# Kernel tuning notes

Measured on AMD Instinct MI355X. Metric: run time of the kernel, lower is better.

The kernel has to match this reference:

```python
import jax, jax.numpy as jnp
import numpy as np

D_HEAD = 64
KV_GROUPS = 3
KSIZE = 7


def _win_idx(L, ksize):
    # NATTEN neighborhood: window centered at i, shifted to stay in-bounds.
    start = jnp.clip(jnp.arange(L) - ksize // 2, 0, L - ksize)  # [L]
    return start[:, None] + jnp.arange(ksize)[None, :]          # [L, k]


def _natten2d(q, k, v, ksize):
    # q,k,v: [n, nh, H, W, e]; q pre-scaled.
    H, W = q.shape[2], q.shape[3]
    ih = _win_idx(H, ksize)  # [H, k]
    iw = _win_idx(W, ksize)  # [W, k]
    # gather per-query key/value windows: [n, nh, H, W, k, k, e]
    kg = k[:, :, ih[:, None, :, None], iw[None, :, None, :], :]
    vg = v[:, :, ih[:, None, :, None], iw[None, :, None, :], :]
    logits = jnp.einsum('nhije,nhijabe->nhijab', q, kg)  # [n,nh,H,W,k,k]
    n_, nh = logits.shape[:2]
    a = jax.nn.softmax(logits.reshape(n_, nh, H, W, ksize * ksize), axis=-1)
    a = a.reshape(logits.shape)
    return jnp.einsum('nhijab,nhijabe->nhije', a, vg)  # [n,nh,H,W,e]


def _to_heads(p, nh, e):
    n, h, w, _ = p.shape
    return p.reshape(n, h, w, nh, e).transpose(0, 3, 1, 2, 4)  # [n,nh,h,w,e]


def setup_inputs() -> dict:
    key = jax.random.key(0)
    k1, k2, k3 = jax.random.split(key, 3)
    x = jax.random.normal(k1, (2, 32, 32, 768), dtype=jnp.float32)
    w_qkv = jax.random.normal(k2, (1280, 768), dtype=jnp.float32) * 0.02
    w_out = jax.random.normal(k3, (768, 768), dtype=jnp.float32) * 0.02
    return {"x": x, "w_qkv": w_qkv, "w_out": w_out}


def reference(x, w_qkv, w_out):
    n, H, W, d_model = x.shape
    q_heads = d_model // D_HEAD
    kv_heads = q_heads // KV_GROUPS
    qkv = x @ w_qkv.T  # [n,H,W,1280]
    q, k, v = jnp.split(
        qkv, [q_heads * D_HEAD, (q_heads + kv_heads) * D_HEAD], axis=-1)
    q = _to_heads(q, q_heads, D_HEAD)
    k = jnp.tile(_to_heads(k, kv_heads, D_HEAD), (1, KV_GROUPS, 1, 1, 1))
    v = jnp.tile(_to_heads(v, kv_heads, D_HEAD), (1, KV_GROUPS, 1, 1, 1))
    q = q / (D_HEAD ** 0.5)
    o = _natten2d(q, k, v, KSIZE)           # [n,nh,H,W,e]
    o = o.transpose(0, 2, 3, 1, 4).reshape(n, H, W, d_model)
    return o @ w_out.T
```

## Files before the change

### kernel.cpp

```cpp
#include <hip/hip_runtime.h>
#include <hip/hip_bf16.h>


typedef __attribute__((ext_vector_type(8))) __bf16 bf16x8;
typedef __attribute__((ext_vector_type(4))) float floatx4;
typedef unsigned short u16;

__device__ inline u16 f2bf(float f) {
    union { float f; unsigned u; } v; v.f = f;
    return (u16)((v.u + 0x7fff + ((v.u >> 16) & 1)) >> 16);
}

__device__ inline void gl_lds16(const void* g, void* l) {
    __builtin_amdgcn_global_load_lds(
        (const __attribute__((address_space(1))) void*)g,
        (__attribute__((address_space(3))) void*)l, 16, 0, 0);
}

__global__ __launch_bounds__(256) void convert_kernel(
    const float* __restrict__ x, const float* __restrict__ w1,
    const float* __restrict__ w2, u16* __restrict__ xb,
    u16* __restrict__ w1b, u16* __restrict__ w2b)
{
    int t = blockIdx.x * blockDim.x + threadIdx.x;
    const float* s; u16* d;
    if (t < 393216)      { s = x;  d = xb; }
    else if (t < 638976) { s = w1; d = w1b; t -= 393216; }
    else                 { s = w2; d = w2b; t -= 638976; }
    float4 v = ((const float4*)s)[t];
    ushort4 o;
    o.x = f2bf(v.x); o.y = f2bf(v.y); o.z = f2bf(v.z); o.w = f2bf(v.w);
    ((ushort4*)d)[t] = o;
}

template<int MODE>
__global__ __launch_bounds__(256) void gemm_nt(
    const u16* __restrict__ A, const u16* __restrict__ B,
    float* __restrict__ out, u16* __restrict__ Cq, u16* __restrict__ vT,
    int K)
{
    __shared__ __align__(16) u16 As[8 * 2048];
    __shared__ __align__(16) u16 Bs[8 * 2048];
    const int tid = threadIdx.x;
    const int lane = tid & 63;
    const int wave = tid >> 6;
    const int bm = blockIdx.y * 64;
    const int bn = blockIdx.x * 64;
    const int qr = (wave >> 1) * 32;
    const int qc = (wave & 1) * 32;

    floatx4 acc[2][2] = {};

    const u16* Xsrc = (wave < 2) ? A : B;
    const int   bx  = (wave < 2) ? bm : bn;
    u16* Xlds       = (wave < 2) ? As : Bs;
    const int half  = wave & 1;
    const int l2 = lane >> 2;
    const int l3 = (lane & 3) * 8;
    int gofs[16], lofs[16];
    #pragma unroll
    for (int cc = 0; cc < 16; cc++) {
        int c = half * 16 + cc, kc = c & 7, rg = c >> 3;
        gofs[cc] = (bx + rg * 16 + l2) * K + kc * 32 + l3;
        lofs[cc] = kc * 2048 + rg * 512;
    }

    const int fr = lane & 15;
    const int fk = (lane >> 4) * 8;

    for (int k0 = 0; k0 < K; k0 += 256) {
        #pragma unroll
        for (int cc = 0; cc < 16; cc++)
            gl_lds16(Xsrc + gofs[cc] + k0, Xlds + lofs[cc]);
        __syncthreads();
        #pragma unroll
        for (int kc = 0; kc < 8; kc++) {
            bf16x8 af0 = *(const bf16x8*)&As[kc * 2048 + (qr +      fr) * 32 + fk];
            bf16x8 af1 = *(const bf16x8*)&As[kc * 2048 + (qr + 16 + fr) * 32 + fk];
            bf16x8 bf0 = *(const bf16x8*)&Bs[kc * 2048 + (qc +      fr) * 32 + fk];
            bf16x8 bf1 = *(const bf16x8*)&Bs[kc * 2048 + (qc + 16 + fr) * 32 + fk];
            acc[0][0] = __builtin_amdgcn_mfma_f32_16x16x32_bf16(af0, bf0, acc[0][0], 0, 0, 0);
            acc[0][1] = __builtin_amdgcn_mfma_f32_16x16x32_bf16(af0, bf1, acc[0][1], 0, 0, 0);
            acc[1][0] = __builtin_amdgcn_mfma_f32_16x16x32_bf16(af1, bf0, acc[1][0], 0, 0, 0);
            acc[1][1] = __builtin_amdgcn_mfma_f32_16x16x32_bf16(af1, bf1, acc[1][1], 0, 0, 0);
        }
        __syncthreads();
    }

    const int cr = (lane >> 4) * 4;
    const int ccol = lane & 15;
    #pragma unroll
    for (int i = 0; i < 2; i++) {
        #pragma unroll
        for (int j = 0; j < 2; j++) {
            const int row0 = bm + qr + i * 16 + cr;
            const int col  = bn + qc + j * 16 + ccol;
            if (MODE == 0) {
                float4 w = {acc[i][j][0], acc[i][j][1], acc[i][j][2], acc[i][j][3]};
                *(float4*)&out[(size_t)col * 768 + row0] = w;
            } else {
                if (row0 < 1024) {
                    ushort4 w;
                    w.x = f2bf(acc[i][j][0]); w.y = f2bf(acc[i][j][1]);
                    w.z = f2bf(acc[i][j][2]); w.w = f2bf(acc[i][j][3]);
                    *(ushort4*)&Cq[(size_t)col * 1024 + row0] = w;
                } else {
                    #pragma unroll
                    for (int r = 0; r < 4; r++)
                        vT[(size_t)(row0 + r - 1024) * 2048 + col] = f2bf(acc[i][j][r]);
                }
            }
        }
    }
}

__global__ __launch_bounds__(256) void natten_mfma(
    const u16* __restrict__ qkv, const u16* __restrict__ vT,
    u16* __restrict__ o)
{
    __shared__ __align__(16) u16 Pw[4 * 512];
    const int h  = blockIdx.x;
    const int tb = blockIdx.y;
    const int g  = h & 3;
    const int batch = tb >> 4;
    const int ti = ((tb >> 2) & 3) * 8;
    const int tj = (tb & 3) * 8;
    const int wu_i = min(max(ti - 3, 0), 18);
    const int oj   = min(max(tj - 3, 0) & ~3, 16);
    const int lane = threadIdx.x & 63, wave = threadIdx.x >> 6;
    const int pixbase = batch << 10;

    const int fr = lane & 15;
    const int fk = (lane >> 4) * 8;

    bf16x8 aq0, aq1;
    {
        int qq = wave * 16 + fr;
        int pixq = pixbase + (ti + (qq >> 3)) * 32 + tj + (qq & 7);
        const u16* qp = &qkv[(size_t)pixq * 1024 + h * 64];
        aq0 = *(const bf16x8*)(qp + fk);
        aq1 = *(const bf16x8*)(qp + 32 + fk);
    }

    bool colok[4]; int tlo[4], thi[4];
    #pragma unroll
    for (int r = 0; r < 4; r++) {
        int qq = wave * 16 + (lane >> 4) * 4 + r;
        int qi = ti + (qq >> 3), qj = tj + (qq & 7);
        int si = min(max(qi - 3, 0), 25);
        int sj = min(max(qj - 3, 0), 25);
        colok[r] = (oj + fr >= sj) && (oj + fr <= sj + 6);
        tlo[r] = si - wu_i; thi[r] = tlo[r] + 6;
    }

    float s[14][4];
    float mx[4] = {-1e30f, -1e30f, -1e30f, -1e30f};
    #pragma unroll
    for (int t = 0; t < 14; t++) {
        int kp = pixbase + (wu_i + t) * 32 + oj + fr;
        const u16* krow = &qkv[(size_t)kp * 1024 + 768 + g * 64];
        bf16x8 bk0 = *(const bf16x8*)(krow + fk);
        bf16x8 bk1 = *(const bf16x8*)(krow + 32 + fk);
        floatx4 a4 = {};
        a4 = __builtin_amdgcn_mfma_f32_16x16x32_bf16(aq0, bk0, a4, 0, 0, 0);
        a4 = __builtin_amdgcn_mfma_f32_16x16x32_bf16(aq1, bk1, a4, 0, 0, 0);
        #pragma unroll
        for (int r = 0; r < 4; r++) {
            bool v = colok[r] && (t >= tlo[r]) && (t <= thi[r]);
            s[t][r] = v ? a4[r] * 0.125f : -1e30f;
            mx[r] = fmaxf(mx[r], s[t][r]);
        }
    }
    #pragma unroll
    for (int r = 0; r < 4; r++) {
        mx[r] = fmaxf(mx[r], __shfl_xor(mx[r], 1));
        mx[r] = fmaxf(mx[r], __shfl_xor(mx[r], 2));
        mx[r] = fmaxf(mx[r], __shfl_xor(mx[r], 4));
        mx[r] = fmaxf(mx[r], __shfl_xor(mx[r], 8));
    }
    float l[4] = {0.f, 0.f, 0.f, 0.f};
    #pragma unroll
    for (int t = 0; t < 14; t++)
        #pragma unroll
        for (int r = 0; r < 4; r++) {
            float p = __expf(s[t][r] - mx[r]);
            s[t][r] = p; l[r] += p;
        }
    #pragma unroll
    for (int r = 0; r < 4; r++) {
        l[r] += __shfl_xor(l[r], 1);
        l[r] += __shfl_xor(l[r], 2);
        l[r] += __shfl_xor(l[r], 4);
        l[r] += __shfl_xor(l[r], 8);
    }
    float rinv[4];
    #pragma unroll
    for (int r = 0; r < 4; r++) rinv[r] = 1.0f / l[r];

    u16* pw = &Pw[wave * 512];
    floatx4 oacc[4] = {};
    const int vrow = (fk >= 16) ? 1 : 0;
    const int vcol = oj + (fk & 8);
    #pragma unroll
    for (int kc = 0; kc < 7; kc++) {
        #pragma unroll
        for (int tt = 0; tt < 2; tt++) {
            int t = kc * 2 + tt;
            #pragma unroll
            for (int r = 0; r < 4; r++)
                pw[((lane >> 4) * 4 + r) * 32 + tt * 16 + fr] =
                    f2bf(s[t][r] * rinv[r]);
        }
        bf16x8 bp = *(const bf16x8*)&pw[fr * 32 + fk];
        const int vpix = pixbase + (wu_i + kc * 2 + vrow) * 32 + vcol;
        #pragma unroll
        for (int u = 0; u < 4; u++) {
            const u16* vp = &vT[(size_t)(g * 64 + u * 16 + fr) * 2048 + vpix];
            union { ushort4 q[2]; bf16x8 v; } av;
            av.q[0] = *(const ushort4*)vp;
            av.q[1] = *(const ushort4*)(vp + 4);
            oacc[u] = __builtin_amdgcn_mfma_f32_16x16x32_bf16(av.v, bp, oacc[u], 0, 0, 0);
        }
    }

    {
        int qq = wave * 16 + fr;
        int pixq = pixbase + (ti + (qq >> 3)) * 32 + tj + (qq & 7);
        u16* op = &o[(size_t)pixq * 768 + h * 64];
        #pragma unroll
        for (int u = 0; u < 4; u++) {
            ushort4 w;
            w.x = f2bf(oacc[u][0]); w.y = f2bf(oacc[u][1]);
            w.z = f2bf(oacc[u][2]); w.w = f2bf(oacc[u][3]);
            *(ushort4*)(op + u * 16 + (lane >> 4) * 4) = w;
        }
    }
}

extern "C" void kernel_launch(void* const* d_in, const int* in_sizes, int n_in,
                              void* d_out, int out_size, void* d_ws, size_t ws_size,
                              hipStream_t stream)
{
    const float* x     = (const float*)d_in[0];
    const float* w_qkv = (const float*)d_in[1];
    const float* w_out = (const float*)d_in[2];
    float* out = (float*)d_out;

    char* ws = (char*)d_ws;
    u16* qkvb = (u16*)ws; ws += (size_t)2048 * 1024 * 2;
    u16* vTb  = (u16*)ws; ws += (size_t)256 * 2048 * 2 + 64;
    u16* xb   = (u16*)ws; ws += (size_t)2048 * 768 * 2;
    u16* w1b  = (u16*)ws; ws += (size_t)1280 * 768 * 2;
    u16* w2b  = (u16*)ws; ws += (size_t)768 * 768 * 2;
    u16* ob   = (u16*)ws;

    convert_kernel<<<dim3(3072), dim3(256), 0, stream>>>(x, w_qkv, w_out, xb, w1b, w2b);

    gemm_nt<1><<<dim3(2048 / 64, 1280 / 64), dim3(256), 0, stream>>>(
        w1b, xb, nullptr, qkvb, vTb, 768);

    natten_mfma<<<dim3(12, 32), dim3(256), 0, stream>>>(qkvb, vTb, ob);

    gemm_nt<0><<<dim3(2048 / 64, 768 / 64), dim3(256), 0, stream>>>(
        w2b, ob, out, nullptr, nullptr, 768);
}
```

Baseline: 104.6 us.

## Replace LDS-staged GEMM with direct global-to-register MFMA fragment loads

Both projection GEMMs drop LDS staging via global_load_lds and the barriers around it. Each wave now loads its bf16 MFMA fragments straight from global memory into registers, with K fixed at compile time and the K loop fully unrolled. This removes LDS traffic and __syncthreads, but the waves of a block no longer share loaded tiles, so global and L2 traffic rises. Each lane also reads 16-byte strided pieces per row, which coalesces less well.

```diff
diff --git a/kernel.cpp b/kernel.cpp
--- a/kernel.cpp
+++ b/kernel.cpp
@@ -9,12 +9,6 @@
 __device__ inline u16 f2bf(float f) {
     union { float f; unsigned u; } v; v.f = f;
     return (u16)((v.u + 0x7fff + ((v.u >> 16) & 1)) >> 16);
-}
-
-__device__ inline void gl_lds16(const void* g, void* l) {
-    __builtin_amdgcn_global_load_lds(
-        (const __attribute__((address_space(1))) void*)g,
-        (__attribute__((address_space(3))) void*)l, 16, 0, 0);
 }
 
 __global__ __launch_bounds__(256) void convert_kernel(
@@ -33,14 +27,11 @@
     ((ushort4*)d)[t] = o;
 }
 
-template<int MODE>
-__global__ __launch_bounds__(256) void gemm_nt(
+template<int MODE, int K>
+__global__ __launch_bounds__(256) void gemm_direct(
     const u16* __restrict__ A, const u16* __restrict__ B,
-    float* __restrict__ out, u16* __restrict__ Cq, u16* __restrict__ vT,
-    int K)
-{
-    __shared__ __align__(16) u16 As[8 * 2048];
-    __shared__ __align__(16) u16 Bs[8 * 2048];
+    float* __restrict__ out, u16* __restrict__ Cq, u16* __restrict__ vT)
+{
     const int tid = threadIdx.x;
     const int lane = tid & 63;
     const int wave = tid >> 6;
@@ -49,42 +40,26 @@
     const int qr = (wave >> 1) * 32;
     const int qc = (wave & 1) * 32;
 
-    floatx4 acc[2][2] = {};
-
-    const u16* Xsrc = (wave < 2) ? A : B;
-    const int   bx  = (wave < 2) ? bm : bn;
-    u16* Xlds       = (wave < 2) ? As : Bs;
-    const int half  = wave & 1;
-    const int l2 = lane >> 2;
-    const int l3 = (lane & 3) * 8;
-    int gofs[16], lofs[16];
-    #pragma unroll
-    for (int cc = 0; cc < 16; cc++) {
-        int c = half * 16 + cc, kc = c & 7, rg = c >> 3;
-        gofs[cc] = (bx + rg * 16 + l2) * K + kc * 32 + l3;
-        lofs[cc] = kc * 2048 + rg * 512;
-    }
-
     const int fr = lane & 15;
     const int fk = (lane >> 4) * 8;
 
-    for (int k0 = 0; k0 < K; k0 += 256) {
-        #pragma unroll
-        for (int cc = 0; cc < 16; cc++)
-            gl_lds16(Xsrc + gofs[cc] + k0, Xlds + lofs[cc]);
-        __syncthreads();
-        #pragma unroll
-        for (int kc = 0; kc < 8; kc++) {
-            bf16x8 af0 = *(const bf16x8*)&As[kc * 2048 + (qr +      fr) * 32 + fk];
-            bf16x8 af1 = *(const bf16x8*)&As[kc * 2048 + (qr + 16 + fr) * 32 + fk];
-            bf16x8 bf0 = *(const bf16x8*)&Bs[kc * 2048 + (qc +      fr) * 32 + fk];
-            bf16x8 bf1 = *(const bf16x8*)&Bs[kc * 2048 + (qc + 16 + fr) * 32 + fk];
-            acc[0][0] = __builtin_amdgcn_mfma_f32_16x16x32_bf16(af0, bf0, acc[0][0], 0, 0, 0);
-            acc[0][1] = __builtin_amdgcn_mfma_f32_16x16x32_bf16(af0, bf1, acc[0][1], 0, 0, 0);
-            acc[1][0] = __builtin_amdgcn_mfma_f32_16x16x32_bf16(af1, bf0, acc[1][0], 0, 0, 0);
-            acc[1][1] = __builtin_amdgcn_mfma_f32_16x16x32_bf16(af1, bf1, acc[1][1], 0, 0, 0);
-        }
-        __syncthreads();
+    const u16* a0 = A + (size_t)(bm + qr + fr)      * K + fk;
+    const u16* a1 = A + (size_t)(bm + qr + 16 + fr) * K + fk;
+    const u16* b0 = B + (size_t)(bn + qc + fr)      * K + fk;
+    const u16* b1 = B + (size_t)(bn + qc + 16 + fr) * K + fk;
+
+    floatx4 acc[2][2] = {};
+
+    #pragma unroll
+    for (int k = 0; k < K; k += 32) {
+        bf16x8 af0 = *(const bf16x8*)(a0 + k);
+        bf16x8 af1 = *(const bf16x8*)(a1 + k);
+        bf16x8 bf0 = *(const bf16x8*)(b0 + k);
+        bf16x8 bf1 = *(const bf16x8*)(b1 + k);
+        acc[0][0] = __builtin_amdgcn_mfma_f32_16x16x32_bf16(af0, bf0, acc[0][0], 0, 0, 0);
+        acc[0][1] = __builtin_amdgcn_mfma_f32_16x16x32_bf16(af0, bf1, acc[0][1], 0, 0, 0);
+        acc[1][0] = __builtin_amdgcn_mfma_f32_16x16x32_bf16(af1, bf0, acc[1][0], 0, 0, 0);
+        acc[1][1] = __builtin_amdgcn_mfma_f32_16x16x32_bf16(af1, bf1, acc[1][1], 0, 0, 0);
     }
 
     const int cr = (lane >> 4) * 4;
@@ -256,11 +231,11 @@
 
     convert_kernel<<<dim3(3072), dim3(256), 0, stream>>>(x, w_qkv, w_out, xb, w1b, w2b);
 
-    gemm_nt<1><<<dim3(2048 / 64, 1280 / 64), dim3(256), 0, stream>>>(
-        w1b, xb, nullptr, qkvb, vTb, 768);
+    gemm_direct<1, 768><<<dim3(2048 / 64, 1280 / 64), dim3(256), 0, stream>>>(
+        w1b, xb, nullptr, qkvb, vTb);
 
     natten_mfma<<<dim3(12, 32), dim3(256), 0, stream>>>(qkvb, vTb, ob);
 
-    gemm_nt<0><<<dim3(2048 / 64, 768 / 64), dim3(256), 0, stream>>>(
-        w2b, ob, out, nullptr, nullptr, 768);
-}
+    gemm_direct<0, 768><<<dim3(2048 / 64, 768 / 64), dim3(256), 0, stream>>>(
+        w2b, ob, out, nullptr, nullptr);
+}
```

Result: slower. 139.9 us (+33.7%).
